# Kernel tuning notes

Measured on AMD Instinct MI355X. Metric: run time of the kernel, lower is better.

## Reference

```python
import jax, jax.numpy as jnp
import numpy as np

TAU = 1.5
SCALE = 0.125
EPS = 1e-5
H = 8

@jax.custom_vjp
def spike(u):
    return (u >= 0.0).astype(u.dtype)

def _spike_fwd(u):
    return spike(u), u

def _spike_bwd(u, g):
    # ATan surrogate gradient, alpha=2 (spikingjelly default)
    return (g / (1.0 + (jnp.pi * u) ** 2),)

spike.defvjp(_spike_fwd, _spike_bwd)

def lif_ms(xt):
    # xt: (T, ...) multi-step LIF, decay_input=True, v_th=1, hard reset to 0, detach_reset
    def step(v, x):
        v = v + (x - v) / TAU
        s = spike(v - 1.0)
        v = v * (1.0 - jax.lax.stop_gradient(s))
        return v, s
    _, s = jax.lax.scan(step, jnp.zeros_like(xt[0]), xt)
    return s

def bn(x, g, b, m, var):
    # eval-mode BatchNorm1d over channel dim of (B, C, L)
    inv = g / jnp.sqrt(var + EPS)
    return (x - m[None, :, None]) * inv[None, :, None] + b[None, :, None]

def setup_inputs() -> dict:
    key = jax.random.key(0)
    ks = jax.random.split(key, 16)
    B, C, T, N = 8, 512, 4, 256
    w_scale = 1.0 / np.sqrt(C)
    inp = {
        'x': jax.random.normal(ks[0], (B, C, T, N), jnp.float32),
        'wq': jax.random.normal(ks[1], (C, C), jnp.float32) * w_scale,
        'wk': jax.random.normal(ks[2], (C, C), jnp.float32) * w_scale,
        'wv': jax.random.normal(ks[3], (C, C), jnp.float32) * w_scale,
        'wp': jax.random.normal(ks[4], (C, C), jnp.float32) * w_scale,
        'bp': jnp.zeros((C,), jnp.float32),
        'gq': jax.random.uniform(ks[5], (C,), jnp.float32, 0.5, 1.5),
        'bq': jax.random.uniform(ks[6], (C,), jnp.float32),
        'mq': jnp.zeros((C,), jnp.float32),
        'vq': jnp.ones((C,), jnp.float32),
        'gk': jax.random.uniform(ks[7], (C,), jnp.float32, 0.5, 1.5),
        'bk': jax.random.uniform(ks[8], (C,), jnp.float32),
        'mk': jnp.zeros((C,), jnp.float32),
        'vk': jnp.ones((C,), jnp.float32),
        'gv': jax.random.uniform(ks[9], (C,), jnp.float32, 0.5, 1.5),
        'bv': jax.random.uniform(ks[10], (C,), jnp.float32),
        'mv': jnp.zeros((C,), jnp.float32),
        'vv': jnp.ones((C,), jnp.float32),
        'gp': jax.random.uniform(ks[11], (C,), jnp.float32, 0.5, 1.5),
        'bpn': jax.random.uniform(ks[12], (C,), jnp.float32),
        'mp': jnp.zeros((C,), jnp.float32),
        'vp': jnp.ones((C,), jnp.float32),
    }
    return inp

def reference(x, wq, wk, wv, wp, bp, gq, bq, mq, vq, gk, bk, mk, vk,
              gv, bv, mv, vv, gp, bpn, mp, vp):
    B, C, T, N = x.shape
    L = T * N
    d = C // H

    # proj_bn then multi-step proj_lif over time dim
    xb = bn(x.reshape(B, C, L), gp, bpn, mp, vp).reshape(B, C, T, N)
    s0 = lif_ms(jnp.transpose(xb, (2, 0, 1, 3)))            # (T,B,C,N)
    x_for_qkv = jnp.transpose(s0, (1, 2, 0, 3)).reshape(B, C, L)  # (B,C,L)

    def qkv_branch(w, g, b_, m, v_):
        y = bn(jnp.einsum('oc,bcl->bol', w, x_for_qkv), g, b_, m, v_)
        y = y.reshape(B, C, T, N)
        sy = lif_ms(jnp.transpose(y, (2, 0, 1, 3)))         # (T,B,C,N)
        sy = jnp.transpose(sy, (1, 0, 3, 2)).reshape(B, L, C)  # (B,T,N,C)->(B,L,C)
        return jnp.transpose(sy.reshape(B, L, H, d), (0, 2, 1, 3))  # (B,H,L,d)

    q = qkv_branch(wq, gq, bq, mq, vq)
    k = qkv_branch(wk, gk, bk, mk, vk)
    v = qkv_branch(wv, gv, bv, mv, vv)

    attn = jnp.einsum('bhqd,bhkd->bhqk', q, k)              # no softmax
    o = jnp.einsum('bhqk,bhkd->bhqd', attn, v) * SCALE
    o = jnp.transpose(o, (0, 1, 3, 2)).reshape(B, C, L)

    # single-step attn_lif: v = o/tau from zero state, spike at threshold 1
    s = spike(o / TAU - 1.0)

    out = jnp.einsum('oc,bcl->bol', wp, s) + bp[None, :, None]
    return out.reshape(B, C, T, N)
```

## Files before the change

kernel.cpp:

```cpp
#include <hip/hip_runtime.h>
#include <hip/hip_bf16.h>


#define NB 8
#define NC 512
#define NT 4
#define NN 256
#define NL 1024
#define NH 8
#define ND 64
#define BCL (NB*NC*NL)

typedef __attribute__((ext_vector_type(8))) short  short8v;
typedef __attribute__((ext_vector_type(8))) unsigned short us8;
typedef __attribute__((ext_vector_type(4))) unsigned short us4;
typedef __attribute__((ext_vector_type(4))) float f32x4;

__device__ __forceinline__ float bu2f(unsigned short u) {
  return __uint_as_float(((unsigned)u) << 16);
}
__device__ __forceinline__ unsigned short f2bu(float f) {
  unsigned b = __float_as_uint(f);
  return (unsigned short)((b + 0x7FFFu + ((b >> 16) & 1u)) >> 16);
}

__global__ void k_prep(const float* __restrict__ wq, const float* __restrict__ wk,
                       const float* __restrict__ wv, const float* __restrict__ wp,
                       const float* __restrict__ x,
                       const float* __restrict__ g,  const float* __restrict__ bt,
                       const float* __restrict__ mu, const float* __restrict__ var,
                       unsigned short* __restrict__ H2,
                       unsigned short* __restrict__ ST0) {
  if (blockIdx.x < 512) {
    int gi = blockIdx.x * 256 + threadIdx.x;
    int p = gi >> 15;
    int o = (gi >> 6) & 511;
    int k8 = gi & 63;
    int rt = o >> 7, r = o & 127;
    int k0i = k8 >> 3, chunk = k8 & 7;
    const float* W = (p == 0) ? wq : (p == 1) ? wk : (p == 2) ? wv : wp;
    const float* src = W + (size_t)o * NC + k8 * 8;
    us8 a[3];
#pragma unroll
    for (int i = 0; i < 8; i++) {
      float w = src[i];
      unsigned short u1 = f2bu(w);
      float r1 = w - bu2f(u1);
      unsigned short u2 = f2bu(r1);
      float r2 = r1 - bu2f(u2);
      unsigned short u3 = f2bu(r2);
      a[0][i] = u1; a[1][i] = u2; a[2][i] = u3;
    }
#pragma unroll
    for (int j = 0; j < 3; j++) {
      size_t off = ((size_t)((((p * 3 + j) * 4 + rt) * 8 + k0i) * 8 + chunk)) * 1024
                   + (size_t)r * 8;
      *(us8*)&H2[off] = a[j];
    }
  } else {
    int bidx = blockIdx.x - 512;
    int b  = bidx >> 6;
    int c0 = (bidx & 63) * 8;
    int n  = threadIdx.x;
    unsigned short spk[NT][8];
#pragma unroll
    for (int i = 0; i < 8; i++) {
      int c = c0 + i;
      float inv = g[c] / sqrtf(var[c] + 1e-5f);
      float m = mu[c], be = bt[c];
      const float* xp = x + ((size_t)(b * NC + c)) * NL + n;
      float v = 0.f;
#pragma unroll
      for (int t = 0; t < NT; t++) {
        float y = (xp[t * NN] - m) * inv + be;
        v = v + (y - v) / 1.5f;
        unsigned short s = 0;
        if (v - 1.0f >= 0.f) { s = 0x3F80; v = 0.f; }
        spk[t][i] = s;
      }
    }
#pragma unroll
    for (int t = 0; t < NT; t++) {
      us8 pk;
#pragma unroll
      for (int i = 0; i < 8; i++) pk[i] = spk[t][i];
      *(us8*)&ST0[((size_t)b * NL + t * NN + n) * NC + c0] = pk;
    }
  }
}

__global__ __launch_bounds__(256) void
k_qkv(const unsigned short* __restrict__ H2,
      const unsigned short* __restrict__ ST0,
      const float* __restrict__ gq, const float* __restrict__ bq,
      const float* __restrict__ mq, const float* __restrict__ vq,
      const float* __restrict__ gk, const float* __restrict__ bk,
      const float* __restrict__ mk, const float* __restrict__ vk,
      const float* __restrict__ gv, const float* __restrict__ bv,
      const float* __restrict__ mv, const float* __restrict__ vv,
      unsigned short* __restrict__ STq, unsigned short* __restrict__ STk,
      unsigned short* __restrict__ STv) {
  __shared__ __align__(16) unsigned short sB[2][128 * 64];

  int id = blockIdx.x;
  int n0 = (id & 7) * 32;
  int rt = (id >> 3) & 3;
  int b  = (id >> 5) & 7;
  int p  = id >> 8;

  int tid = threadIdx.x;
  int w = tid >> 6, lane = tid & 63, quad = lane >> 4, l15 = lane & 15;
  int xorv = l15 & 7;

  const unsigned short* Sb = ST0 + (size_t)b * NL * NC;

  f32x4 acc[2][8];
#pragma unroll
  for (int ri = 0; ri < 2; ri++)
#pragma unroll
    for (int jj = 0; jj < 8; jj++) acc[ri][jj] = (f32x4){0.f, 0.f, 0.f, 0.f};

  us8 breg[4];
  int ccs[4], segs[4];
  size_t bsrc[4];
#pragma unroll
  for (int i = 0; i < 4; i++) {
    int idx = tid + i * 256;
    int cc = idx >> 3, seg = idx & 7;
    int t = (cc >> 4) & 3, nn = (cc & 15) | ((cc >> 6) << 4);
    ccs[i] = cc; segs[i] = seg;
    bsrc[i] = (size_t)(t * NN + n0 + nn) * NC + seg * 8;
  }
#pragma unroll
  for (int i = 0; i < 4; i++) breg[i] = *(const us8*)&Sb[bsrc[i]];
#pragma unroll
  for (int i = 0; i < 4; i++)
    *(us8*)&sB[0][ccs[i] * 64 + ((segs[i] ^ (ccs[i] & 7)) << 3)] = breg[i];

  for (int k0i = 0; k0i < 8; k0i++) {
    __syncthreads();
    int buf = k0i & 1;
    if (k0i < 7) {
#pragma unroll
      for (int i = 0; i < 4; i++)
        breg[i] = *(const us8*)&Sb[bsrc[i] + (size_t)(k0i + 1) * 64];
    }
#pragma unroll
    for (int ks = 0; ks < 2; ks++) {
      int c8 = ks * 4 + quad;
      int poff = (c8 ^ xorv) << 3;
      short8v bf[8];
#pragma unroll
      for (int jj = 0; jj < 8; jj++)
        bf[jj] = *(const short8v*)&sB[buf][(jj * 16 + l15) * 64 + poff];
#pragma unroll
      for (int j = 0; j < 3; j++) {
        const unsigned short* Hj =
            H2 + ((size_t)(((p * 3 + j) * 4 + rt) * 8 + k0i)) * 8192
               + (size_t)c8 * 1024;
        short8v a0 = *(const short8v*)&Hj[(w * 32 + l15) * 8];
        short8v a1 = *(const short8v*)&Hj[(w * 32 + 16 + l15) * 8];
#pragma unroll
        for (int jj = 0; jj < 8; jj++) {
          acc[0][jj] = __builtin_amdgcn_mfma_f32_16x16x32_bf16(a0, bf[jj], acc[0][jj], 0, 0, 0);
          acc[1][jj] = __builtin_amdgcn_mfma_f32_16x16x32_bf16(a1, bf[jj], acc[1][jj], 0, 0, 0);
        }
      }
    }
    if (k0i < 7) {
#pragma unroll
      for (int i = 0; i < 4; i++)
        *(us8*)&sB[buf ^ 1][ccs[i] * 64 + ((segs[i] ^ (ccs[i] & 7)) << 3)] = breg[i];
    }
  }

  const float *g, *bb, *mm, *vr;
  unsigned short* So;
  if (p == 0)      { g = gq; bb = bq; mm = mq; vr = vq; So = STq; }
  else if (p == 1) { g = gk; bb = bk; mm = mk; vr = vk; So = STk; }
  else             { g = gv; bb = bv; mm = mv; vr = vv; So = STv; }
  So += (size_t)b * NL * NC;

#pragma unroll
  for (int ri = 0; ri < 2; ri++) {
    int ob = rt * 128 + w * 32 + ri * 16 + quad * 4;
    float av[4], mvv[4], bvv[4];
#pragma unroll
    for (int r = 0; r < 4; r++) {
      av[r]  = g[ob + r] / sqrtf(vr[ob + r] + 1e-5f);
      mvv[r] = mm[ob + r];
      bvv[r] = bb[ob + r];
    }
#pragma unroll
    for (int nh = 0; nh < 2; nh++) {
      int n = n0 + (nh << 4) + l15;
      unsigned short sp[4][4];
#pragma unroll
      for (int r = 0; r < 4; r++) {
        float vmem = 0.f;
#pragma unroll
        for (int t = 0; t < NT; t++) {
          float y = (acc[ri][nh * 4 + t][r] - mvv[r]) * av[r] + bvv[r];
          vmem = vmem + (y - vmem) / 1.5f;
          unsigned short s = 0;
          if (vmem - 1.0f >= 0.f) { s = 0x3F80; vmem = 0.f; }
          sp[t][r] = s;
        }
      }
#pragma unroll
      for (int t = 0; t < NT; t++) {
        us4 pk;
#pragma unroll
        for (int r = 0; r < 4; r++) pk[r] = sp[t][r];
        *(us4*)&So[(size_t)(t * NN + n) * NC + ob] = pk;
      }
    }
  }
}

__global__ void k_kvM(const unsigned short* __restrict__ STk,
                      const unsigned short* __restrict__ STv,
                      float* __restrict__ Mpart) {
  int bh = blockIdx.x, ch = blockIdx.y;
  int b = bh >> 3, h = bh & 7;
  const unsigned short* Kp = STk + (size_t)b * NL * NC + h * ND;
  const unsigned short* Vp = STv + (size_t)b * NL * NC + h * ND;
  __shared__ float sK[64][72];
  __shared__ float sV[64][72];
  int tid = threadIdx.x, tx = tid & 15, ty = tid >> 4;
  float acc[4][4] = {};
  for (int lt = 0; lt < 2; lt++) {
    int lb = ch * 128 + lt * 64;
#pragma unroll
    for (int i = 0; i < 2; i++) {
      int idx = tid + i * 256;
      int r = idx >> 3, seg = idx & 7;
      us8 kv = *(const us8*)&Kp[(size_t)(lb + r) * NC + seg * 8];
      us8 vv = *(const us8*)&Vp[(size_t)(lb + r) * NC + seg * 8];
#pragma unroll
      for (int q2 = 0; q2 < 8; q2++) {
        sK[r][seg * 8 + q2] = bu2f(kv[q2]);
        sV[r][seg * 8 + q2] = bu2f(vv[q2]);
      }
    }
    __syncthreads();
#pragma unroll 8
    for (int lc = 0; lc < 64; lc++) {
      float kvx[4], vvx[4];
#pragma unroll
      for (int i = 0; i < 4; i++) kvx[i] = sK[lc][ty * 4 + i];
#pragma unroll
      for (int j2 = 0; j2 < 4; j2++) vvx[j2] = sV[lc][tx * 4 + j2];
#pragma unroll
      for (int i = 0; i < 4; i++)
#pragma unroll
        for (int j2 = 0; j2 < 4; j2++)
          acc[i][j2] += kvx[i] * vvx[j2];
    }
    __syncthreads();
  }
  float* Mp = Mpart + ((size_t)ch * 64 + bh) * 4096;
#pragma unroll
  for (int i = 0; i < 4; i++) {
    float4 v4 = make_float4(acc[i][0], acc[i][1], acc[i][2], acc[i][3]);
    *(float4*)&Mp[(ty * 4 + i) * ND + tx * 4] = v4;
  }
}

__global__ __launch_bounds__(256) void
k_attn(const unsigned short* __restrict__ STq,
       const float* __restrict__ Mpart,
       unsigned short* __restrict__ STs) {
  __shared__ unsigned short MT1[64 * 64];
  __shared__ unsigned short MT2[64 * 64];
  int lt = blockIdx.x, bh = blockIdx.y;
  int b = bh >> 3, h = bh & 7;
  int tid = threadIdx.x;
  int w = tid >> 6, lane = tid & 63, quad = lane >> 4, l15 = lane & 15;

#pragma unroll
  for (int i = 0; i < 4; i++) {
    int idx4 = tid + i * 256;
    float4 s = ((const float4*)Mpart)[(size_t)bh * 1024 + idx4];
#pragma unroll
    for (int ch = 1; ch < 8; ch++) {
      float4 t = ((const float4*)Mpart)[((size_t)ch * 64 + bh) * 1024 + idx4];
      s.x += t.x; s.y += t.y; s.z += t.z; s.w += t.w;
    }
    int e = idx4 >> 4;
    int dd0 = (idx4 * 4) & 63;
    int chunk = e >> 3;
    float sv[4] = {s.x, s.y, s.z, s.w};
#pragma unroll
    for (int r = 0; r < 4; r++) {
      int dd = dd0 + r;
      unsigned short u1 = f2bu(sv[r]);
      unsigned short u2 = f2bu(sv[r] - bu2f(u1));
      int pos = dd * 64 + (((chunk ^ (dd & 7)) << 3) | (e & 7));
      MT1[pos] = u1;
      MT2[pos] = u2;
    }
  }
  __syncthreads();

  const unsigned short* Qp = STq + (size_t)b * NL * NC + h * ND;
  int lbase = lt * 256 + w * 64;

  f32x4 acc[4][4];
#pragma unroll
  for (int dt = 0; dt < 4; dt++)
#pragma unroll
    for (int j = 0; j < 4; j++) acc[dt][j] = (f32x4){0.f, 0.f, 0.f, 0.f};

#pragma unroll
  for (int ks = 0; ks < 2; ks++) {
    short8v bq[4];
#pragma unroll
    for (int ltile = 0; ltile < 4; ltile++)
      bq[ltile] = *(const short8v*)&Qp[(size_t)(lbase + ltile * 16 + l15) * NC
                                       + ks * 32 + quad * 8];
    int c8 = ks * 4 + quad;
#pragma unroll
    for (int dt = 0; dt < 4; dt++) {
      int dd = dt * 16 + l15;
      int off = dd * 64 + ((c8 ^ (dd & 7)) << 3);
      short8v a1 = *(const short8v*)&MT1[off];
      short8v a2 = *(const short8v*)&MT2[off];
#pragma unroll
      for (int ltile = 0; ltile < 4; ltile++) {
        acc[dt][ltile] = __builtin_amdgcn_mfma_f32_16x16x32_bf16(a1, bq[ltile], acc[dt][ltile], 0, 0, 0);
        acc[dt][ltile] = __builtin_amdgcn_mfma_f32_16x16x32_bf16(a2, bq[ltile], acc[dt][ltile], 0, 0, 0);
      }
    }
  }

  unsigned short* Sp = STs + (size_t)b * NL * NC + h * ND;
#pragma unroll
  for (int dt = 0; dt < 4; dt++)
#pragma unroll
    for (int ltile = 0; ltile < 4; ltile++) {
      int l = lbase + ltile * 16 + l15;
      int dd = dt * 16 + quad * 4;
      us4 pk;
#pragma unroll
      for (int r = 0; r < 4; r++) pk[r] = (acc[dt][ltile][r] >= 12.0f) ? 0x3F80 : 0;
      *(us4*)&Sp[(size_t)l * NC + dd] = pk;
    }
}

__global__ __launch_bounds__(256) void
k_out(const unsigned short* __restrict__ H2,
      const unsigned short* __restrict__ STs,
      const float* __restrict__ bp, float* __restrict__ out) {
  __shared__ __align__(16) unsigned short sB[2][64 * 64];

  int id = blockIdx.x;
  int l0 = (id & 15) * 64;
  int rt = (id >> 4) & 3;
  int b  = id >> 6;

  int tid = threadIdx.x;
  int w = tid >> 6, lane = tid & 63, quad = lane >> 4, l15 = lane & 15;
  int xorv = l15 & 7;

  const unsigned short* Sb = STs + (size_t)b * NL * NC;

  f32x4 acc[2][4];
#pragma unroll
  for (int ri = 0; ri < 2; ri++)
#pragma unroll
    for (int jj = 0; jj < 4; jj++) acc[ri][jj] = (f32x4){0.f, 0.f, 0.f, 0.f};

  us8 breg[2];
  int ccs[2], segs[2];
  size_t bsrc[2];
#pragma unroll
  for (int i = 0; i < 2; i++) {
    int idx = tid + i * 256;
    int cc = idx >> 3, seg = idx & 7;
    ccs[i] = cc; segs[i] = seg;
    bsrc[i] = (size_t)(l0 + cc) * NC + seg * 8;
  }
#pragma unroll
  for (int i = 0; i < 2; i++) breg[i] = *(const us8*)&Sb[bsrc[i]];
#pragma unroll
  for (int i = 0; i < 2; i++)
    *(us8*)&sB[0][ccs[i] * 64 + ((segs[i] ^ (ccs[i] & 7)) << 3)] = breg[i];

  for (int k0i = 0; k0i < 8; k0i++) {
    __syncthreads();
    int buf = k0i & 1;
    if (k0i < 7) {
#pragma unroll
      for (int i = 0; i < 2; i++)
        breg[i] = *(const us8*)&Sb[bsrc[i] + (size_t)(k0i + 1) * 64];
    }
#pragma unroll
    for (int ks = 0; ks < 2; ks++) {
      int c8 = ks * 4 + quad;
      int poff = (c8 ^ xorv) << 3;
      short8v bf[4];
#pragma unroll
      for (int jj = 0; jj < 4; jj++)
        bf[jj] = *(const short8v*)&sB[buf][(jj * 16 + l15) * 64 + poff];
#pragma unroll
      for (int j = 0; j < 3; j++) {
        const unsigned short* Hj =
            H2 + ((size_t)(((9 + j) * 4 + rt) * 8 + k0i)) * 8192
               + (size_t)c8 * 1024;
        short8v a0 = *(const short8v*)&Hj[(w * 32 + l15) * 8];
        short8v a1 = *(const short8v*)&Hj[(w * 32 + 16 + l15) * 8];
#pragma unroll
        for (int jj = 0; jj < 4; jj++) {
          acc[0][jj] = __builtin_amdgcn_mfma_f32_16x16x32_bf16(a0, bf[jj], acc[0][jj], 0, 0, 0);
          acc[1][jj] = __builtin_amdgcn_mfma_f32_16x16x32_bf16(a1, bf[jj], acc[1][jj], 0, 0, 0);
        }
      }
    }
    if (k0i < 7) {
#pragma unroll
      for (int i = 0; i < 2; i++)
        *(us8*)&sB[buf ^ 1][ccs[i] * 64 + ((segs[i] ^ (ccs[i] & 7)) << 3)] = breg[i];
    }
  }

#pragma unroll
  for (int ri = 0; ri < 2; ri++) {
    int ob = rt * 128 + w * 32 + ri * 16 + quad * 4;
#pragma unroll
    for (int jj = 0; jj < 4; jj++) {
      int l = l0 + jj * 16 + l15;
#pragma unroll
      for (int r = 0; r < 4; r++)
        out[((size_t)(b * NC + ob + r)) * NL + l] = acc[ri][jj][r] + bp[ob + r];
    }
  }
}

extern "C" void kernel_launch(void* const* d_in, const int* in_sizes, int n_in,
                              void* d_out, int out_size, void* d_ws, size_t ws_size,
                              hipStream_t stream) {
  (void)in_sizes; (void)n_in; (void)out_size; (void)ws_size;
  const float* x   = (const float*)d_in[0];
  const float* wq  = (const float*)d_in[1];
  const float* wk  = (const float*)d_in[2];
  const float* wv  = (const float*)d_in[3];
  const float* wp  = (const float*)d_in[4];
  const float* bp  = (const float*)d_in[5];
  const float* gq  = (const float*)d_in[6];
  const float* bq  = (const float*)d_in[7];
  const float* mq  = (const float*)d_in[8];
  const float* vq  = (const float*)d_in[9];
  const float* gk  = (const float*)d_in[10];
  const float* bk  = (const float*)d_in[11];
  const float* mk  = (const float*)d_in[12];
  const float* vk  = (const float*)d_in[13];
  const float* gv  = (const float*)d_in[14];
  const float* bv  = (const float*)d_in[15];
  const float* mv  = (const float*)d_in[16];
  const float* vvv = (const float*)d_in[17];
  const float* gp  = (const float*)d_in[18];
  const float* bpn = (const float*)d_in[19];
  const float* mp  = (const float*)d_in[20];
  const float* vp  = (const float*)d_in[21];

  unsigned short* H2  = (unsigned short*)d_ws;
  unsigned short* ST0 = H2 + (size_t)4 * 3 * NC * NC;
  unsigned short* STq = ST0 + BCL;
  unsigned short* STk = STq + BCL;
  unsigned short* STv = STk + BCL;
  unsigned short* STs = STv + BCL;
  float* Mpart = (float*)(STs + BCL);

  dim3 blk(256);
  k_prep<<<1024, blk, 0, stream>>>(wq, wk, wv, wp, x, gp, bpn, mp, vp, H2, ST0);
  k_qkv<<<768, blk, 0, stream>>>(H2, ST0,
      gq, bq, mq, vq, gk, bk, mk, vk, gv, bv, mv, vvv, STq, STk, STv);
  k_kvM<<<dim3(64, 8), blk, 0, stream>>>(STk, STv, Mpart);
  k_attn<<<dim3(4, 64), blk, 0, stream>>>(STq, Mpart, STs);
  k_out<<<512, blk, 0, stream>>>(H2, STs, bp, (float*)d_out);
}
```

Measured before the change: 198.8 us.

## Switch QKV and output GEMMs to 32x32x16 MFMA with repacked weight layout

Replaces the 16x16x32 bf16 MFMA tiles in the QKV and output projection kernels with 32x32x16 MFMA, repacking the split-bf16 weight buffer so each wave loads one 32-row A fragment per k-step. This is meant to reduce the number of MFMA issues and A-fragment loads per unit of work and to improve operand reuse. The shared-memory B tile ordering and the epilogue lane-to-row mapping are rewritten to match the 32x32 accumulator layout, which adds register pressure from the larger accumulators.

```diff
diff --git a/kernel.cpp b/kernel.cpp
--- a/kernel.cpp
+++ b/kernel.cpp
@@ -15,6 +15,7 @@
 typedef __attribute__((ext_vector_type(8))) unsigned short us8;
 typedef __attribute__((ext_vector_type(4))) unsigned short us4;
 typedef __attribute__((ext_vector_type(4))) float f32x4;
+typedef __attribute__((ext_vector_type(16))) float f32x16;
 
 __device__ __forceinline__ float bu2f(unsigned short u) {
   return __uint_as_float(((unsigned)u) << 16);
@@ -29,15 +30,17 @@
                        const float* __restrict__ x,
                        const float* __restrict__ g,  const float* __restrict__ bt,
                        const float* __restrict__ mu, const float* __restrict__ var,
-                       unsigned short* __restrict__ H2,
+                       unsigned short* __restrict__ H3,
                        unsigned short* __restrict__ ST0) {
   if (blockIdx.x < 512) {
     int gi = blockIdx.x * 256 + threadIdx.x;
     int p = gi >> 15;
     int o = (gi >> 6) & 511;
     int k8 = gi & 63;
-    int rt = o >> 7, r = o & 127;
-    int k0i = k8 >> 3, chunk = k8 & 7;
+    int rt32 = o >> 5, lrow = o & 31;
+    int k0i = k8 >> 3, kk = k8 & 7;
+    int kstep = kk >> 1, khalf = kk & 1;
+    int ln = khalf * 32 + lrow;
     const float* W = (p == 0) ? wq : (p == 1) ? wk : (p == 2) ? wv : wp;
     const float* src = W + (size_t)o * NC + k8 * 8;
     us8 a[3];
@@ -53,9 +56,9 @@
     }
 #pragma unroll
     for (int j = 0; j < 3; j++) {
-      size_t off = ((size_t)((((p * 3 + j) * 4 + rt) * 8 + k0i) * 8 + chunk)) * 1024
-                   + (size_t)r * 8;
-      *(us8*)&H2[off] = a[j];
+      size_t off = ((size_t)((((p * 3 + j) * 16 + rt32) * 8 + k0i) * 4 + kstep)) * 512
+                   + (size_t)ln * 8;
+      *(us8*)&H3[off] = a[j];
     }
   } else {
     int bidx = blockIdx.x - 512;
@@ -90,7 +93,7 @@
 }
 
 __global__ __launch_bounds__(256) void
-k_qkv(const unsigned short* __restrict__ H2,
+k_qkv(const unsigned short* __restrict__ H3,
       const unsigned short* __restrict__ ST0,
       const float* __restrict__ gq, const float* __restrict__ bq,
       const float* __restrict__ mq, const float* __restrict__ vq,
@@ -109,16 +112,16 @@
   int p  = id >> 8;
 
   int tid = threadIdx.x;
-  int w = tid >> 6, lane = tid & 63, quad = lane >> 4, l15 = lane & 15;
-  int xorv = l15 & 7;
+  int w = tid >> 6, lane = tid & 63;
+  int l31 = lane & 31, h = lane >> 5;
 
   const unsigned short* Sb = ST0 + (size_t)b * NL * NC;
 
-  f32x4 acc[2][8];
-#pragma unroll
-  for (int ri = 0; ri < 2; ri++)
-#pragma unroll
-    for (int jj = 0; jj < 8; jj++) acc[ri][jj] = (f32x4){0.f, 0.f, 0.f, 0.f};
+  f32x16 acc[4];
+#pragma unroll
+  for (int t4 = 0; t4 < 4; t4++)
+#pragma unroll
+    for (int r = 0; r < 16; r++) acc[t4][r] = 0.f;
 
   us8 breg[4];
   int ccs[4], segs[4];
@@ -127,7 +130,7 @@
   for (int i = 0; i < 4; i++) {
     int idx = tid + i * 256;
     int cc = idx >> 3, seg = idx & 7;
-    int t = (cc >> 4) & 3, nn = (cc & 15) | ((cc >> 6) << 4);
+    int t = cc >> 5, nn = cc & 31;
     ccs[i] = cc; segs[i] = seg;
     bsrc[i] = (size_t)(t * NN + n0 + nn) * NC + seg * 8;
   }
@@ -146,25 +149,22 @@
         breg[i] = *(const us8*)&Sb[bsrc[i] + (size_t)(k0i + 1) * 64];
     }
 #pragma unroll
-    for (int ks = 0; ks < 2; ks++) {
-      int c8 = ks * 4 + quad;
-      int poff = (c8 ^ xorv) << 3;
-      short8v bf[8];
-#pragma unroll
-      for (int jj = 0; jj < 8; jj++)
-        bf[jj] = *(const short8v*)&sB[buf][(jj * 16 + l15) * 64 + poff];
+    for (int kstep = 0; kstep < 4; kstep++) {
+      int c8 = kstep * 2 + h;
+      short8v bf[4];
+#pragma unroll
+      for (int t4 = 0; t4 < 4; t4++) {
+        int cc = t4 * 32 + l31;
+        bf[t4] = *(const short8v*)&sB[buf][cc * 64 + ((c8 ^ (cc & 7)) << 3)];
+      }
 #pragma unroll
       for (int j = 0; j < 3; j++) {
         const unsigned short* Hj =
-            H2 + ((size_t)(((p * 3 + j) * 4 + rt) * 8 + k0i)) * 8192
-               + (size_t)c8 * 1024;
-        short8v a0 = *(const short8v*)&Hj[(w * 32 + l15) * 8];
-        short8v a1 = *(const short8v*)&Hj[(w * 32 + 16 + l15) * 8];
-#pragma unroll
-        for (int jj = 0; jj < 8; jj++) {
-          acc[0][jj] = __builtin_amdgcn_mfma_f32_16x16x32_bf16(a0, bf[jj], acc[0][jj], 0, 0, 0);
-          acc[1][jj] = __builtin_amdgcn_mfma_f32_16x16x32_bf16(a1, bf[jj], acc[1][jj], 0, 0, 0);
-        }
+            H3 + ((size_t)((((p * 3 + j) * 16 + rt * 4 + w) * 8 + k0i) * 4 + kstep)) * 512;
+        short8v a = *(const short8v*)&Hj[lane * 8];
+#pragma unroll
+        for (int t4 = 0; t4 < 4; t4++)
+          acc[t4] = __builtin_amdgcn_mfma_f32_32x32x16_bf16(a, bf[t4], acc[t4], 0, 0, 0);
       }
     }
     if (k0i < 7) {
@@ -181,39 +181,36 @@
   else             { g = gv; bb = bv; mm = mv; vr = vv; So = STv; }
   So += (size_t)b * NL * NC;
 
-#pragma unroll
-  for (int ri = 0; ri < 2; ri++) {
-    int ob = rt * 128 + w * 32 + ri * 16 + quad * 4;
+  int n = n0 + l31;
+#pragma unroll
+  for (int grp = 0; grp < 4; grp++) {
+    int ob = rt * 128 + w * 32 + 8 * grp + 4 * h;
     float av[4], mvv[4], bvv[4];
 #pragma unroll
-    for (int r = 0; r < 4; r++) {
-      av[r]  = g[ob + r] / sqrtf(vr[ob + r] + 1e-5f);
-      mvv[r] = mm[ob + r];
-      bvv[r] = bb[ob + r];
-    }
-#pragma unroll
-    for (int nh = 0; nh < 2; nh++) {
-      int n = n0 + (nh << 4) + l15;
-      unsigned short sp[4][4];
-#pragma unroll
-      for (int r = 0; r < 4; r++) {
-        float vmem = 0.f;
-#pragma unroll
-        for (int t = 0; t < NT; t++) {
-          float y = (acc[ri][nh * 4 + t][r] - mvv[r]) * av[r] + bvv[r];
-          vmem = vmem + (y - vmem) / 1.5f;
-          unsigned short s = 0;
-          if (vmem - 1.0f >= 0.f) { s = 0x3F80; vmem = 0.f; }
-          sp[t][r] = s;
-        }
-      }
+    for (int rr = 0; rr < 4; rr++) {
+      av[rr]  = g[ob + rr] / sqrtf(vr[ob + rr] + 1e-5f);
+      mvv[rr] = mm[ob + rr];
+      bvv[rr] = bb[ob + rr];
+    }
+    unsigned short sp[4][4];
+#pragma unroll
+    for (int rr = 0; rr < 4; rr++) {
+      float vmem = 0.f;
 #pragma unroll
       for (int t = 0; t < NT; t++) {
-        us4 pk;
-#pragma unroll
-        for (int r = 0; r < 4; r++) pk[r] = sp[t][r];
-        *(us4*)&So[(size_t)(t * NN + n) * NC + ob] = pk;
-      }
+        float y = (acc[t][grp * 4 + rr] - mvv[rr]) * av[rr] + bvv[rr];
+        vmem = vmem + (y - vmem) / 1.5f;
+        unsigned short s = 0;
+        if (vmem - 1.0f >= 0.f) { s = 0x3F80; vmem = 0.f; }
+        sp[t][rr] = s;
+      }
+    }
+#pragma unroll
+    for (int t = 0; t < NT; t++) {
+      us4 pk;
+#pragma unroll
+      for (int rr = 0; rr < 4; rr++) pk[rr] = sp[t][rr];
+      *(us4*)&So[(size_t)(t * NN + n) * NC + ob] = pk;
     }
   }
 }
@@ -349,7 +346,7 @@
 }
 
 __global__ __launch_bounds__(256) void
-k_out(const unsigned short* __restrict__ H2,
+k_out(const unsigned short* __restrict__ H3,
       const unsigned short* __restrict__ STs,
       const float* __restrict__ bp, float* __restrict__ out) {
   __shared__ __align__(16) unsigned short sB[2][64 * 64];
@@ -360,16 +357,16 @@
   int b  = id >> 6;
 
   int tid = threadIdx.x;
-  int w = tid >> 6, lane = tid & 63, quad = lane >> 4, l15 = lane & 15;
-  int xorv = l15 & 7;
+  int w = tid >> 6, lane = tid & 63;
+  int l31 = lane & 31, h = lane >> 5;
 
   const unsigned short* Sb = STs + (size_t)b * NL * NC;
 
-  f32x4 acc[2][4];
-#pragma unroll
-  for (int ri = 0; ri < 2; ri++)
-#pragma unroll
-    for (int jj = 0; jj < 4; jj++) acc[ri][jj] = (f32x4){0.f, 0.f, 0.f, 0.f};
+  f32x16 acc[2];
+#pragma unroll
+  for (int j2 = 0; j2 < 2; j2++)
+#pragma unroll
+    for (int r = 0; r < 16; r++) acc[j2][r] = 0.f;
 
   us8 breg[2];
   int ccs[2], segs[2];
@@ -396,25 +393,22 @@
         breg[i] = *(const us8*)&Sb[bsrc[i] + (size_t)(k0i + 1) * 64];
     }
 #pragma unroll
-    for (int ks = 0; ks < 2; ks++) {
-      int c8 = ks * 4 + quad;
-      int poff = (c8 ^ xorv) << 3;
-      short8v bf[4];
-#pragma unroll
-      for (int jj = 0; jj < 4; jj++)
-        bf[jj] = *(const short8v*)&sB[buf][(jj * 16 + l15) * 64 + poff];
+    for (int kstep = 0; kstep < 4; kstep++) {
+      int c8 = kstep * 2 + h;
+      short8v bf[2];
+#pragma unroll
+      for (int j2 = 0; j2 < 2; j2++) {
+        int cc = j2 * 32 + l31;
+        bf[j2] = *(const short8v*)&sB[buf][cc * 64 + ((c8 ^ (cc & 7)) << 3)];
+      }
 #pragma unroll
       for (int j = 0; j < 3; j++) {
         const unsigned short* Hj =
-            H2 + ((size_t)(((9 + j) * 4 + rt) * 8 + k0i)) * 8192
-               + (size_t)c8 * 1024;
-        short8v a0 = *(const short8v*)&Hj[(w * 32 + l15) * 8];
-        short8v a1 = *(const short8v*)&Hj[(w * 32 + 16 + l15) * 8];
-#pragma unroll
-        for (int jj = 0; jj < 4; jj++) {
-          acc[0][jj] = __builtin_amdgcn_mfma_f32_16x16x32_bf16(a0, bf[jj], acc[0][jj], 0, 0, 0);
-          acc[1][jj] = __builtin_amdgcn_mfma_f32_16x16x32_bf16(a1, bf[jj], acc[1][jj], 0, 0, 0);
-        }
+            H3 + ((size_t)((((9 + j) * 16 + rt * 4 + w) * 8 + k0i) * 4 + kstep)) * 512;
+        short8v a = *(const short8v*)&Hj[lane * 8];
+#pragma unroll
+        for (int j2 = 0; j2 < 2; j2++)
+          acc[j2] = __builtin_amdgcn_mfma_f32_32x32x16_bf16(a, bf[j2], acc[j2], 0, 0, 0);
       }
     }
     if (k0i < 7) {
@@ -425,14 +419,14 @@
   }
 
 #pragma unroll
-  for (int ri = 0; ri < 2; ri++) {
-    int ob = rt * 128 + w * 32 + ri * 16 + quad * 4;
-#pragma unroll
-    for (int jj = 0; jj < 4; jj++) {
-      int l = l0 + jj * 16 + l15;
-#pragma unroll
-      for (int r = 0; r < 4; r++)
-        out[((size_t)(b * NC + ob + r)) * NL + l] = acc[ri][jj][r] + bp[ob + r];
+  for (int grp = 0; grp < 4; grp++) {
+    int ob = rt * 128 + w * 32 + 8 * grp + 4 * h;
+#pragma unroll
+    for (int j2 = 0; j2 < 2; j2++) {
+      int l = l0 + j2 * 32 + l31;
+#pragma unroll
+      for (int rr = 0; rr < 4; rr++)
+        out[((size_t)(b * NC + ob + rr)) * NL + l] = acc[j2][grp * 4 + rr] + bp[ob + rr];
     }
   }
 }
@@ -464,8 +458,8 @@
   const float* mp  = (const float*)d_in[20];
   const float* vp  = (const float*)d_in[21];
 
-  unsigned short* H2  = (unsigned short*)d_ws;
-  unsigned short* ST0 = H2 + (size_t)4 * 3 * NC * NC;
+  unsigned short* H3  = (unsigned short*)d_ws;
+  unsigned short* ST0 = H3 + (size_t)4 * 3 * NC * NC;
   unsigned short* STq = ST0 + BCL;
   unsigned short* STk = STq + BCL;
   unsigned short* STv = STk + BCL;
@@ -473,10 +467,10 @@
   float* Mpart = (float*)(STs + BCL);
 
   dim3 blk(256);
-  k_prep<<<1024, blk, 0, stream>>>(wq, wk, wv, wp, x, gp, bpn, mp, vp, H2, ST0);
-  k_qkv<<<768, blk, 0, stream>>>(H2, ST0,
+  k_prep<<<1024, blk, 0, stream>>>(wq, wk, wv, wp, x, gp, bpn, mp, vp, H3, ST0);
+  k_qkv<<<768, blk, 0, stream>>>(H3, ST0,
       gq, bq, mq, vq, gk, bk, mk, vk, gv, bv, mv, vvv, STq, STk, STv);
   k_kvM<<<dim3(64, 8), blk, 0, stream>>>(STk, STv, Mpart);
   k_attn<<<dim3(4, 64), blk, 0, stream>>>(STq, Mpart, STs);
-  k_out<<<512, blk, 0, stream>>>(H2, STs, bp, (float*)d_out);
-}
+  k_out<<<512, blk, 0, stream>>>(H3, STs, bp, (float*)d_out);
+}
```

New measurement: 197.5 us. About the same (-0.7%).
